# Performance work log

Hardware: AMD Instinct MI355X
Metric: run time of the kernel (lower is better)

The kernel has to match this reference:

```python
import jax, jax.numpy as jnp
import numpy as np

NUM_PAIRS, PAIR_DIM, MACRO_DIM, NUM_SLOTS, BATCH = 28, 128, 256, 64, 4096
D_ALL = NUM_PAIRS * PAIR_DIM  # 3584
EPS = 1e-5


def _layernorm(x, g, b):
    mu = jnp.mean(x, axis=-1, keepdims=True)
    var = jnp.mean(jnp.square(x - mu), axis=-1, keepdims=True)
    return (x - mu) * jax.lax.rsqrt(var + EPS) * g + b


def _memory_read(q, keys, values):
    # attention-style associative read: softmax(q K^T / sqrt(dk)) V
    dk = keys.shape[-1]
    scores = jnp.einsum('bd,sd->bs', q, keys) / jnp.sqrt(jnp.asarray(dk, q.dtype))
    attn = jax.nn.softmax(scores, axis=-1)
    return jnp.einsum('bs,sv->bv', attn, values)


def setup_inputs() -> dict:
    key = jax.random.key(0)
    ks = jax.random.split(key, 12)
    s = lambda k, shape, scale=0.02: jax.random.normal(k, shape, dtype=jnp.float32) * scale
    return {
        'pair_states': jax.random.normal(ks[0], (BATCH, NUM_PAIRS, PAIR_DIM), dtype=jnp.float32),
        'macro_state': jax.random.normal(ks[1], (BATCH, MACRO_DIM), dtype=jnp.float32),
        'mem_pair_keys': s(ks[2], (NUM_SLOTS, PAIR_DIM)),
        'mem_pair_vals': s(ks[3], (NUM_SLOTS, D_ALL)),
        'mem_macro_keys': s(ks[4], (NUM_SLOTS, MACRO_DIM)),
        'mem_macro_vals': s(ks[5], (NUM_SLOTS, D_ALL)),
        'fusion_w1': s(ks[6], (2 * D_ALL, D_ALL)),
        'fusion_b1': jnp.zeros((D_ALL,), jnp.float32),
        'fusion_ln_g': jnp.ones((D_ALL,), jnp.float32),
        'fusion_ln_b': jnp.zeros((D_ALL,), jnp.float32),
        'fusion_w2': s(ks[7], (D_ALL, D_ALL)),
        'fusion_b2': jnp.zeros((D_ALL,), jnp.float32),
        'pair_w': s(ks[8], (NUM_PAIRS, 2 * PAIR_DIM, PAIR_DIM)),
        'pair_b': jnp.zeros((NUM_PAIRS, PAIR_DIM), jnp.float32),
        'pair_ln_g': jnp.ones((NUM_PAIRS, PAIR_DIM), jnp.float32),
        'pair_ln_b': jnp.zeros((NUM_PAIRS, PAIR_DIM), jnp.float32),
    }


def reference(pair_states, macro_state, mem_pair_keys, mem_pair_vals,
              mem_macro_keys, mem_macro_vals, fusion_w1, fusion_b1,
              fusion_ln_g, fusion_ln_b, fusion_w2, fusion_b2,
              pair_w, pair_b, pair_ln_g, pair_ln_b):
    B = pair_states.shape[0]
    # associative memory reads
    pair_query = jnp.mean(pair_states, axis=1)                       # (B, pair_dim)
    pair_corr = _memory_read(pair_query, mem_pair_keys, mem_pair_vals)   # (B, D_ALL)
    macro_corr = _memory_read(macro_state, mem_macro_keys, mem_macro_vals)  # (B, D_ALL)
    # fusion MLP: Linear -> LayerNorm -> GELU -> Linear
    h = jnp.concatenate([pair_corr, macro_corr], axis=-1) @ fusion_w1 + fusion_b1
    h = jax.nn.gelu(_layernorm(h, fusion_ln_g, fusion_ln_b), approximate=False)
    fused = (h @ fusion_w2 + fusion_b2).reshape(B, NUM_PAIRS, PAIR_DIM)
    # per-pair Linear + LayerNorm, batched over the pair axis
    x = jnp.concatenate([pair_states, fused], axis=-1)               # (B, P, 2*pair_dim)
    out = jnp.einsum('bpd,pde->bpe', x, pair_w) + pair_b
    return _layernorm(out, pair_ln_g, pair_ln_b)
```

## Files before the change

### kernel.cpp

```cpp
#include <hip/hip_runtime.h>
#include <hip/hip_bf16.h>
#include <math.h>


#define B_SZ  4096
#define NPAIR 28
#define PDIM  128
#define MDIM  256
#define NSLOT 64
#define DALL  3584
#define DCAT  7168
#define KS2   16
#define KCH2  448

typedef __hip_bfloat16 bf16;
typedef __attribute__((ext_vector_type(8))) short bf16x8;
typedef __attribute__((ext_vector_type(4))) short short4v;
typedef __attribute__((ext_vector_type(4))) float f32x4;

#define BARRIER() asm volatile("s_barrier" ::: "memory")
#define LGKM0()   asm volatile("s_waitcnt lgkmcnt(0)" ::: "memory")
#define VMCNT4()  asm volatile("s_waitcnt vmcnt(4)" ::: "memory")
#define VMCNT0()  asm volatile("s_waitcnt vmcnt(0)" ::: "memory")

__device__ __forceinline__ void async_copy16(void* lds, const void* g) {
  __builtin_amdgcn_global_load_lds((__attribute__((address_space(1))) void*)g,
                                   (__attribute__((address_space(3))) void*)lds,
                                   16, 0, 0);
}

__global__ __launch_bounds__(512, 2)
void gemm224(const bf16* __restrict__ A, const bf16* __restrict__ Bt,
             bf16* __restrict__ Cout, const float* __restrict__ bias) {
  __shared__ __align__(16) char smem[131072];
  const int tid = threadIdx.x;
  const int wid = tid >> 6, lane = tid & 63;
  const int lr = lane & 15, lk = lane >> 4;
  const int wm = wid >> 1, wn = wid & 1;
  const int swz = ((int)blockIdx.x & 7) * 32 + ((int)blockIdx.x >> 3);
  const int bx = swz & 15, by = swz >> 4;
  const int col0 = bx * 224, row0 = by * 256;

  char* sA = smem;
  char* sB = smem + 65536;

  const int srow = tid >> 3;
  const int sg = (tid & 7) ^ (srow & 7);
  const bf16* aStage = A + (long)(row0 + srow) * DALL + sg * 8;
  const bf16* bStage = Bt + (long)(col0 + srow) * DALL + sg * 8;
  const int wOff = wid << 10;

  const int NT = DALL >> 6;

  const int sx = lr & 7;
  const int arowb = wm * 64 + lr;
  const int browb = wn * 112 + lr;

  f32x4 acc[4][7];
  const f32x4 zero = {0.f, 0.f, 0.f, 0.f};
#pragma unroll
  for (int m = 0; m < 4; ++m)
#pragma unroll
    for (int n = 0; n < 7; ++n) acc[m][n] = zero;

#pragma unroll
  for (int i = 0; i < 4; ++i)
    async_copy16(sB + i * 8192 + wOff, bStage + (long)i * 64 * DALL);
#pragma unroll
  for (int i = 0; i < 4; ++i)
    async_copy16(sA + i * 8192 + wOff, aStage + (long)i * 64 * DALL);
#pragma unroll
  for (int i = 0; i < 4; ++i)
    async_copy16(sB + 32768 + i * 8192 + wOff, bStage + (long)i * 64 * DALL + 64);
  VMCNT4();
  BARRIER();

  bf16x8 af[4][2], bf[7][2];

  for (int t = 0; t < NT; ++t) {
    const int cur = t & 1;
    char* cA = sA + cur * 32768;
    char* cB = sB + cur * 32768;
    char* nA = sA + (cur ^ 1) * 32768;

    if (t + 1 < NT) {
      const bf16* g = aStage + (long)(t + 1) * 64;
#pragma unroll
      for (int i = 0; i < 4; ++i)
        async_copy16(nA + i * 8192 + wOff, g + (long)i * 64 * DALL);
    }
#pragma unroll
    for (int m = 0; m < 4; ++m)
#pragma unroll
      for (int kk = 0; kk < 2; ++kk)
        af[m][kk] = *(const bf16x8*)(cA + (arowb + m * 16) * 128 +
                                     ((((kk << 2) | lk) ^ sx) << 4));
#pragma unroll
    for (int n = 0; n < 7; ++n)
#pragma unroll
      for (int kk = 0; kk < 2; ++kk)
        bf[n][kk] = *(const bf16x8*)(cB + (browb + n * 16) * 128 +
                                     ((((kk << 2) | lk) ^ sx) << 4));
    __builtin_amdgcn_s_setprio(1);
#pragma unroll
    for (int m = 0; m < 4; ++m)
#pragma unroll
      for (int n = 0; n < 4; ++n)
#pragma unroll
        for (int kk = 0; kk < 2; ++kk)
          acc[m][n] = __builtin_amdgcn_mfma_f32_16x16x32_bf16(
              af[m][kk], bf[n][kk], acc[m][n], 0, 0, 0);
    __builtin_amdgcn_s_setprio(0);
    LGKM0();
    BARRIER();

    const int more = (t + 2 < NT);
    if (more) {
      const bf16* g = bStage + (long)(t + 2) * 64;
#pragma unroll
      for (int i = 0; i < 4; ++i)
        async_copy16(cB + i * 8192 + wOff, g + (long)i * 64 * DALL);
    }
    __builtin_amdgcn_s_setprio(1);
#pragma unroll
    for (int m = 0; m < 4; ++m)
#pragma unroll
      for (int n = 4; n < 7; ++n)
#pragma unroll
        for (int kk = 0; kk < 2; ++kk)
          acc[m][n] = __builtin_amdgcn_mfma_f32_16x16x32_bf16(
              af[m][kk], bf[n][kk], acc[m][n], 0, 0, 0);
    __builtin_amdgcn_s_setprio(0);
    if (more) { VMCNT4(); } else { VMCNT0(); }
    BARRIER();
  }

#pragma unroll
  for (int m = 0; m < 4; ++m) {
#pragma unroll
    for (int n = 0; n < 7; ++n) {
      const int gc = col0 + wn * 112 + n * 16 + lr;
      const float bia = bias[gc];
#pragma unroll
      for (int j = 0; j < 4; ++j) {
        const int gr = row0 + wm * 64 + m * 16 + lk * 4 + j;
        Cout[(long)gr * DALL + gc] = __float2bfloat16(acc[m][n][j] + bia);
      }
    }
  }
}

__global__ __launch_bounds__(256)
void tconv_kernel(const float* __restrict__ in, bf16* __restrict__ out,
                  int R, int C, int inBatch, int outBatch) {
  __shared__ float tile[32][33];
  const int tid = threadIdx.x;
  const int tx = tid & 31, ty = tid >> 5;
  const long ib = (long)blockIdx.z * inBatch;
  const long ob = (long)blockIdx.z * outBatch;
  const int c0 = blockIdx.x * 32, r0 = blockIdx.y * 32;
#pragma unroll
  for (int i = 0; i < 4; ++i)
    tile[ty + i * 8][tx] = in[ib + (long)(r0 + ty + i * 8) * C + c0 + tx];
  __syncthreads();
  const int cl = tid >> 3, rq = (tid & 7) * 4;
  union { bf16 h[4]; short4v v; } u;
#pragma unroll
  for (int j = 0; j < 4; ++j) u.h[j] = __float2bfloat16(tile[rq + j][cl]);
  *(short4v*)(out + ob + (long)(c0 + cl) * R + r0 + rq) = u.v;
}

__global__ __launch_bounds__(256)
void conv2_kernel(const float* __restrict__ pv, const float* __restrict__ mv,
                  bf16* __restrict__ pvb, bf16* __restrict__ mvb) {
  const float* in = blockIdx.y ? mv : pv;
  bf16* out = blockIdx.y ? mvb : pvb;
  const int i = (blockIdx.x * 256 + threadIdx.x) * 8;
  float4 a = *(const float4*)(in + i);
  float4 b = *(const float4*)(in + i + 4);
  union { bf16 h[8]; bf16x8 v; } u;
  u.h[0] = __float2bfloat16(a.x); u.h[1] = __float2bfloat16(a.y);
  u.h[2] = __float2bfloat16(a.z); u.h[3] = __float2bfloat16(a.w);
  u.h[4] = __float2bfloat16(b.x); u.h[5] = __float2bfloat16(b.y);
  u.h[6] = __float2bfloat16(b.z); u.h[7] = __float2bfloat16(b.w);
  *(bf16x8*)(out + i) = u.v;
}

__global__ __launch_bounds__(256)
void prep_kernel(const float* __restrict__ ps, const float* __restrict__ mac,
                 const float* __restrict__ pkeys, const float* __restrict__ mkeys,
                 bf16* __restrict__ psb, bf16* __restrict__ att) {
  const int b = blockIdx.x, tid = threadIdx.x;
  __shared__ float q[PDIM];
  __shared__ float mrow[MDIM];
  __shared__ float red[16][PDIM];
  const float* prow = ps + (long)b * DALL;
  if (tid < MDIM) mrow[tid] = mac[(long)b * MDIM + tid];
  float a8[8];
#pragma unroll
  for (int j = 0; j < 8; ++j) a8[j] = 0.f;
  for (int i = tid * 8; i < DALL; i += 2048) {
    float4 a = *(const float4*)(prow + i);
    float4 c = *(const float4*)(prow + i + 4);
    union { bf16 h[8]; bf16x8 v; } u;
    u.h[0] = __float2bfloat16(a.x); u.h[1] = __float2bfloat16(a.y);
    u.h[2] = __float2bfloat16(a.z); u.h[3] = __float2bfloat16(a.w);
    u.h[4] = __float2bfloat16(c.x); u.h[5] = __float2bfloat16(c.y);
    u.h[6] = __float2bfloat16(c.z); u.h[7] = __float2bfloat16(c.w);
    *(bf16x8*)(psb + (long)b * DALL + i) = u.v;
    a8[0] += a.x; a8[1] += a.y; a8[2] += a.z; a8[3] += a.w;
    a8[4] += c.x; a8[5] += c.y; a8[6] += c.z; a8[7] += c.w;
  }
  {
    float* rp = &red[tid >> 4][(tid & 15) * 8];
    *(f32x4*)rp = *(f32x4*)&a8[0];
    *(f32x4*)(rp + 4) = *(f32x4*)&a8[4];
  }
  __syncthreads();
  if (tid < PDIM) {
    float s = 0.f;
#pragma unroll
    for (int k = 0; k < 16; ++k) s += red[k][tid];
    q[tid] = s * (1.f / NPAIR);
  }
  __syncthreads();
  const int wid = tid >> 6, lane = tid & 63;
  if (wid == 0) {
    float sc = 0.f;
    const float* kr = pkeys + lane * PDIM;
    for (int d = 0; d < PDIM; ++d) sc += q[d] * kr[d];
    sc *= 0.08838834764831845f;
    float mx = sc;
#pragma unroll
    for (int m = 32; m; m >>= 1) mx = fmaxf(mx, __shfl_xor(mx, m));
    float e = expf(sc - mx);
    float ssum = e;
#pragma unroll
    for (int m = 32; m; m >>= 1) ssum += __shfl_xor(ssum, m);
    att[(long)b * 128 + lane] = __float2bfloat16(e / ssum);
  } else if (wid == 1) {
    float sc = 0.f;
    const float* kr = mkeys + lane * MDIM;
    for (int d = 0; d < MDIM; ++d) sc += mrow[d] * kr[d];
    sc *= 0.0625f;
    float mx = sc;
#pragma unroll
    for (int m = 32; m; m >>= 1) mx = fmaxf(mx, __shfl_xor(mx, m));
    float e = expf(sc - mx);
    float ssum = e;
#pragma unroll
    for (int m = 32; m; m >>= 1) ssum += __shfl_xor(ssum, m);
    att[(long)b * 128 + 64 + lane] = __float2bfloat16(e / ssum);
  }
}

__global__ __launch_bounds__(256)
void precompute_direct(const float* __restrict__ w1, const bf16* __restrict__ pvb,
                       const bf16* __restrict__ mvb, float* __restrict__ part) {
  __shared__ __align__(16) bf16 sAt[256 * 40];
  __shared__ __align__(16) bf16 sBt[64 * 32];
  const int tid = threadIdx.x, wid = tid >> 6, lane = tid & 63;
  const int lr = lane & 15, lk = lane >> 4;
  const int n0 = blockIdx.x * 256;
  const int ksb = blockIdx.y;
  const int kbase = ksb * KCH2;
  const bf16* vb = (ksb < 8) ? pvb : mvb;
  const int kcol0 = (ksb < 8) ? kbase : kbase - DALL;

  const int bs = tid >> 2;
  const int bgs = (tid & 3) ^ (bs & 3);

  f32x4 acc[4][4];
  const f32x4 zero = {0.f, 0.f, 0.f, 0.f};
#pragma unroll
  for (int m = 0; m < 4; ++m)
#pragma unroll
    for (int n = 0; n < 4; ++n) acc[m][n] = zero;

  for (int kt = 0; kt < KCH2; kt += 32) {
    __syncthreads();
    {
      const float* src = w1 + (long)(kbase + kt) * DALL + n0 + tid;
      bf16* dst = sAt + tid * 40;
#pragma unroll
      for (int r8 = 0; r8 < 32; r8 += 4) {
        union { bf16 h[4]; short4v v; } u;
#pragma unroll
        for (int j = 0; j < 4; ++j)
          u.h[j] = __float2bfloat16(src[(long)(r8 + j) * DALL]);
        *(short4v*)(dst + r8) = u.v;
      }
    }
    async_copy16((char*)sBt + tid * 16,
                 vb + (long)bs * DALL + kcol0 + kt + bgs * 8);
    __syncthreads();
    bf16x8 af[4], bfr[4];
#pragma unroll
    for (int m = 0; m < 4; ++m)
      af[m] = *(const bf16x8*)((const char*)sAt +
                               ((wid * 64 + m * 16 + lr) * 40 + lk * 8) * 2);
#pragma unroll
    for (int n = 0; n < 4; ++n) {
      const int s = n * 16 + lr;
      bfr[n] = *(const bf16x8*)((const char*)sBt + s * 64 + ((lk ^ (s & 3)) << 4));
    }
#pragma unroll
    for (int m = 0; m < 4; ++m)
#pragma unroll
      for (int n = 0; n < 4; ++n)
        acc[m][n] =
            __builtin_amdgcn_mfma_f32_16x16x32_bf16(af[m], bfr[n], acc[m][n], 0, 0, 0);
  }
#pragma unroll
  for (int m = 0; m < 4; ++m)
#pragma unroll
    for (int n = 0; n < 4; ++n)
#pragma unroll
      for (int j = 0; j < 4; ++j) {
        const int gn = n0 + wid * 64 + m * 16 + lk * 4 + j;
        const int s = n * 16 + lr;
        part[((long)ksb * DALL + gn) * 64 + s] = acc[m][n][j];
      }
}

__global__ __launch_bounds__(256)
void reduce_cvt(const float* __restrict__ part, bf16* __restrict__ cvt) {
  const long i4 = ((long)blockIdx.x * 256 + threadIdx.x) * 4;
  const int n = (int)(i4 >> 7), sc = (int)(i4 & 127);
  const int half = sc >> 6, s0 = sc & 63;
  f32x4 s = {0.f, 0.f, 0.f, 0.f};
#pragma unroll
  for (int j = 0; j < 8; ++j)
    s += *(const f32x4*)(part + ((long)(half * 8 + j) * DALL + n) * 64 + s0);
#pragma unroll
  for (int k = 0; k < 4; ++k) cvt[i4 + k] = __float2bfloat16(s[k]);
}

__global__ __launch_bounds__(256)
void gemm_thin(const bf16* __restrict__ att, const bf16* __restrict__ cvt,
               bf16* __restrict__ hpre, const float* __restrict__ bias) {
  __shared__ __align__(16) bf16 sA[128 * 64];
  __shared__ __align__(16) bf16 sB[128 * 64];
  const int tid = threadIdx.x, wid = tid >> 6, lane = tid & 63;
  const int lr = lane & 15, lk = lane >> 4;
  const int col0 = blockIdx.x * 128, row0 = blockIdx.y * 128;
  const int srl = lane >> 3;
  const int sgl = (lane & 7) ^ srl;
  const int sx = lr & 7;

  f32x4 acc[2][8];
  const f32x4 zero = {0.f, 0.f, 0.f, 0.f};
#pragma unroll
  for (int m = 0; m < 2; ++m)
#pragma unroll
    for (int n = 0; n < 8; ++n) acc[m][n] = zero;

  for (int kt = 0; kt < 2; ++kt) {
    __syncthreads();
#pragma unroll
    for (int i = 0; i < 4; ++i) {
      const int r = i * 32 + wid * 8 + srl;
      async_copy16((char*)sA + i * 4096 + wid * 1024,
                   att + (long)(row0 + r) * 128 + kt * 64 + sgl * 8);
      async_copy16((char*)sB + i * 4096 + wid * 1024,
                   cvt + (long)(col0 + r) * 128 + kt * 64 + sgl * 8);
    }
    __syncthreads();
#pragma unroll
    for (int kk = 0; kk < 2; ++kk) {
      bf16x8 a0[2], b0[8];
      const int gb = (((kk << 2) | lk) ^ sx) << 4;
#pragma unroll
      for (int m = 0; m < 2; ++m)
        a0[m] = *(const bf16x8*)((const char*)sA + (wid * 32 + m * 16 + lr) * 128 + gb);
#pragma unroll
      for (int n = 0; n < 8; ++n)
        b0[n] = *(const bf16x8*)((const char*)sB + (n * 16 + lr) * 128 + gb);
#pragma unroll
      for (int m = 0; m < 2; ++m)
#pragma unroll
        for (int n = 0; n < 8; ++n)
          acc[m][n] = __builtin_amdgcn_mfma_f32_16x16x32_bf16(
              a0[m], b0[n], acc[m][n], 0, 0, 0);
    }
  }
#pragma unroll
  for (int m = 0; m < 2; ++m) {
#pragma unroll
    for (int n = 0; n < 8; ++n) {
      const int gc = col0 + n * 16 + lr;
      const float bia = bias[gc];
#pragma unroll
      for (int j = 0; j < 4; ++j) {
        const int gr = row0 + wid * 32 + m * 16 + lk * 4 + j;
        hpre[(long)gr * DALL + gc] = __float2bfloat16(acc[m][n][j] + bia);
      }
    }
  }
}

__global__ __launch_bounds__(256)
void ln_gelu_kernel(const bf16* __restrict__ h, const float* __restrict__ g,
                    const float* __restrict__ bb, bf16* __restrict__ h2) {
  const int row = blockIdx.x, tid = threadIdx.x;
  const bf16* x = h + (long)row * DALL;
  float v[14];
  float s1 = 0.f, s2 = 0.f;
#pragma unroll
  for (int i = 0; i < 14; ++i) {
    v[i] = __bfloat162float(x[i * 256 + tid]);
    s1 += v[i];
    s2 += v[i] * v[i];
  }
#pragma unroll
  for (int m = 32; m; m >>= 1) {
    s1 += __shfl_xor(s1, m);
    s2 += __shfl_xor(s2, m);
  }
  __shared__ float r1[4], r2[4];
  const int wid = tid >> 6, lane = tid & 63;
  if (lane == 0) {
    r1[wid] = s1;
    r2[wid] = s2;
  }
  __syncthreads();
  s1 = r1[0] + r1[1] + r1[2] + r1[3];
  s2 = r2[0] + r2[1] + r2[2] + r2[3];
  const float mean = s1 * (1.f / DALL);
  const float var = s2 * (1.f / DALL) - mean * mean;
  const float rstd = rsqrtf(var + 1e-5f);
#pragma unroll
  for (int i = 0; i < 14; ++i) {
    const int c = i * 256 + tid;
    const float y = (v[i] - mean) * rstd * g[c] + bb[c];
    const float ge = 0.5f * y * (1.f + erff(y * 0.7071067811865475f));
    h2[(long)row * DALL + c] = __float2bfloat16(ge);
  }
}

__global__ __launch_bounds__(256)
void pair_final(const bf16* __restrict__ psb, const bf16* __restrict__ fusedb,
                const bf16* __restrict__ pwT, const float* __restrict__ pb,
                const float* __restrict__ lng, const float* __restrict__ lnb,
                float* __restrict__ out) {
  __shared__ __align__(16) bf16 sA[128 * 64];
  __shared__ __align__(16) bf16 sB[128 * 64];
  const int tid = threadIdx.x, wid = tid >> 6, lane = tid & 63;
  const int lr = lane & 15, lk = lane >> 4;
  const int p = blockIdx.y, row0 = blockIdx.x * 128;
  const int srl = lane >> 3;
  const int sgl = (lane & 7) ^ srl;
  const int sx = lr & 7;
  const bf16* pwp = pwT + (long)p * (PDIM * MDIM);

  f32x4 acc[2][8];
  const f32x4 zero = {0.f, 0.f, 0.f, 0.f};
#pragma unroll
  for (int m = 0; m < 2; ++m)
#pragma unroll
    for (int n = 0; n < 8; ++n) acc[m][n] = zero;

  for (int kt = 0; kt < 4; ++kt) {
    __syncthreads();
    const bf16* Asrc = (kt < 2) ? psb : fusedb;
    const int acol = p * PDIM + (kt & 1) * 64;
#pragma unroll
    for (int i = 0; i < 4; ++i) {
      const int r = i * 32 + wid * 8 + srl;
      async_copy16((char*)sA + i * 4096 + wid * 1024,
                   Asrc + (long)(row0 + r) * DALL + acol + sgl * 8);
      async_copy16((char*)sB + i * 4096 + wid * 1024,
                   pwp + (long)r * MDIM + kt * 64 + sgl * 8);
    }
    __syncthreads();
#pragma unroll
    for (int kk = 0; kk < 2; ++kk) {
      bf16x8 a0[2], b0[8];
      const int gb = (((kk << 2) | lk) ^ sx) << 4;
#pragma unroll
      for (int m = 0; m < 2; ++m)
        a0[m] = *(const bf16x8*)((const char*)sA + (wid * 32 + m * 16 + lr) * 128 + gb);
#pragma unroll
      for (int n = 0; n < 8; ++n)
        b0[n] = *(const bf16x8*)((const char*)sB + (n * 16 + lr) * 128 + gb);
#pragma unroll
      for (int m = 0; m < 2; ++m)
#pragma unroll
        for (int n = 0; n < 8; ++n)
          acc[m][n] = __builtin_amdgcn_mfma_f32_16x16x32_bf16(
              a0[m], b0[n], acc[m][n], 0, 0, 0);
    }
  }
  float g_[8], b_[8], pb_[8];
#pragma unroll
  for (int n = 0; n < 8; ++n) {
    const int c = n * 16 + lr;
    g_[n] = lng[p * PDIM + c];
    b_[n] = lnb[p * PDIM + c];
    pb_[n] = pb[p * PDIM + c];
  }
#pragma unroll
  for (int m = 0; m < 2; ++m) {
#pragma unroll
    for (int j = 0; j < 4; ++j) {
      float vv[8];
      float s1 = 0.f, s2 = 0.f;
#pragma unroll
      for (int n = 0; n < 8; ++n) {
        vv[n] = acc[m][n][j] + pb_[n];
        s1 += vv[n];
        s2 += vv[n] * vv[n];
      }
#pragma unroll
      for (int msk = 1; msk <= 8; msk <<= 1) {
        s1 += __shfl_xor(s1, msk);
        s2 += __shfl_xor(s2, msk);
      }
      const float mean = s1 * (1.f / 128.f);
      const float var = s2 * (1.f / 128.f) - mean * mean;
      const float rstd = rsqrtf(var + 1e-5f);
      const int gr = row0 + wid * 32 + m * 16 + lk * 4 + j;
      float* orow = out + ((long)gr * NPAIR + p) * PDIM;
#pragma unroll
      for (int n = 0; n < 8; ++n)
        orow[n * 16 + lr] = (vv[n] - mean) * rstd * g_[n] + b_[n];
    }
  }
}

extern "C" void kernel_launch(void* const* d_in, const int* in_sizes, int n_in,
                              void* d_out, int out_size, void* d_ws, size_t ws_size,
                              hipStream_t stream) {
  (void)in_sizes; (void)n_in; (void)out_size; (void)ws_size;
  const float* ps   = (const float*)d_in[0];
  const float* mac  = (const float*)d_in[1];
  const float* pkey = (const float*)d_in[2];
  const float* pval = (const float*)d_in[3];
  const float* mkey = (const float*)d_in[4];
  const float* mval = (const float*)d_in[5];
  const float* w1   = (const float*)d_in[6];
  const float* b1   = (const float*)d_in[7];
  const float* lng1 = (const float*)d_in[8];
  const float* lnb1 = (const float*)d_in[9];
  const float* w2   = (const float*)d_in[10];
  const float* b2   = (const float*)d_in[11];
  const float* pw   = (const float*)d_in[12];
  const float* pb   = (const float*)d_in[13];
  const float* plng = (const float*)d_in[14];
  const float* plnb = (const float*)d_in[15];
  float* out = (float*)d_out;

  char* w = (char*)d_ws;
  size_t off = 0;
  auto carve = [&](size_t bytes) {
    char* pp = w + off;
    off += (bytes + 255) & ~(size_t)255;
    return pp;
  };
  bf16* psb   = (bf16*)carve((size_t)B_SZ * DALL * 2);
  bf16* w2t   = (bf16*)carve((size_t)(DALL + 32) * DALL * 2);
  bf16* pvb   = (bf16*)carve((size_t)NSLOT * DALL * 2);
  bf16* mvb   = (bf16*)carve((size_t)NSLOT * DALL * 2);
  bf16* pwTb  = (bf16*)carve((size_t)NPAIR * PDIM * MDIM * 2);
  bf16* att   = (bf16*)carve((size_t)B_SZ * 128 * 2);
  bf16* cvt   = (bf16*)carve((size_t)DALL * 128 * 2);
  float* part = (float*)carve((size_t)KS2 * DALL * 64 * 4);
  bf16* hpreb = (bf16*)carve((size_t)B_SZ * DALL * 2);
  bf16* h2    = (bf16*)carve((size_t)B_SZ * DALL * 2);
  bf16* fusedb = hpreb;

  conv2_kernel<<<dim3(NSLOT * DALL / 2048, 2), 256, 0, stream>>>(pval, mval, pvb, mvb);
  tconv_kernel<<<dim3(DALL / 32, DALL / 32, 1), 256, 0, stream>>>(w2, w2t, DALL, DALL, 0, 0);
  tconv_kernel<<<dim3(PDIM / 32, MDIM / 32, NPAIR), 256, 0, stream>>>(
      pw, pwTb, MDIM, PDIM, MDIM * PDIM, MDIM * PDIM);
  prep_kernel<<<dim3(B_SZ), 256, 0, stream>>>(ps, mac, pkey, mkey, psb, att);
  precompute_direct<<<dim3(DALL / 256, KS2), 256, 0, stream>>>(w1, pvb, mvb, part);
  reduce_cvt<<<dim3(DALL * 128 / 1024), 256, 0, stream>>>(part, cvt);
  gemm_thin<<<dim3(DALL / 128, B_SZ / 128), 256, 0, stream>>>(att, cvt, hpreb, b1);
  ln_gelu_kernel<<<dim3(B_SZ), 256, 0, stream>>>(hpreb, lng1, lnb1, h2);
  gemm224<<<dim3(256), 512, 0, stream>>>(h2, w2t, fusedb, b2);
  pair_final<<<dim3(B_SZ / 128, NPAIR), 256, 0, stream>>>(
      psb, fusedb, pwTb, pb, plng, plnb, out);
}
```

Before: 280.3 us.

## Fuse thin GEMM with LayerNorm and GELU in one row-block kernel

Merges the K=128 thin GEMM and the LayerNorm+GELU pass into one kernel. Each block owns 16 rows, computes all 3584 columns with MFMA straight from global-memory fragments, stages the pre-activation in about 115 KB of LDS, then normalizes and writes h2. This removes the write and re-read of the 4096x3584 bf16 pre-activation and one kernel launch. In exchange it uses large LDS per block (low occupancy), only 256 blocks, and reloads the cvt matrix from global for every block without LDS staging.

```diff
diff --git a/kernel.cpp b/kernel.cpp
--- a/kernel.cpp
+++ b/kernel.cpp
@@ -12,6 +12,7 @@
 #define DCAT  7168
 #define KS2   16
 #define KCH2  448
+#define HCOLS 3600
 
 typedef __hip_bfloat16 bf16;
 typedef __attribute__((ext_vector_type(8))) short bf16x8;
@@ -337,104 +338,94 @@
 }
 
 __global__ __launch_bounds__(256)
-void gemm_thin(const bf16* __restrict__ att, const bf16* __restrict__ cvt,
-               bf16* __restrict__ hpre, const float* __restrict__ bias) {
-  __shared__ __align__(16) bf16 sA[128 * 64];
-  __shared__ __align__(16) bf16 sB[128 * 64];
+void fused_mlp1(const bf16* __restrict__ att, const bf16* __restrict__ cvt,
+                const float* __restrict__ b1, const float* __restrict__ g,
+                const float* __restrict__ bb, bf16* __restrict__ h2) {
+  __shared__ __align__(16) bf16 sH[16 * HCOLS];
+  __shared__ float sred[4][16][2];
   const int tid = threadIdx.x, wid = tid >> 6, lane = tid & 63;
   const int lr = lane & 15, lk = lane >> 4;
-  const int col0 = blockIdx.x * 128, row0 = blockIdx.y * 128;
-  const int srl = lane >> 3;
-  const int sgl = (lane & 7) ^ srl;
-  const int sx = lr & 7;
-
-  f32x4 acc[2][8];
+  const int r0 = blockIdx.x * 16;
+  const int c0 = wid * 896;
+
+  bf16x8 af[4];
+#pragma unroll
+  for (int ks = 0; ks < 4; ++ks)
+    af[ks] = *(const bf16x8*)(att + (long)(r0 + lr) * 128 + ks * 32 + lk * 8);
+
+  float s1[4], s2[4];
+#pragma unroll
+  for (int j = 0; j < 4; ++j) { s1[j] = 0.f; s2[j] = 0.f; }
+
   const f32x4 zero = {0.f, 0.f, 0.f, 0.f};
 #pragma unroll
-  for (int m = 0; m < 2; ++m)
-#pragma unroll
-    for (int n = 0; n < 8; ++n) acc[m][n] = zero;
-
-  for (int kt = 0; kt < 2; ++kt) {
-    __syncthreads();
-#pragma unroll
-    for (int i = 0; i < 4; ++i) {
-      const int r = i * 32 + wid * 8 + srl;
-      async_copy16((char*)sA + i * 4096 + wid * 1024,
-                   att + (long)(row0 + r) * 128 + kt * 64 + sgl * 8);
-      async_copy16((char*)sB + i * 4096 + wid * 1024,
-                   cvt + (long)(col0 + r) * 128 + kt * 64 + sgl * 8);
-    }
-    __syncthreads();
-#pragma unroll
-    for (int kk = 0; kk < 2; ++kk) {
-      bf16x8 a0[2], b0[8];
-      const int gb = (((kk << 2) | lk) ^ sx) << 4;
-#pragma unroll
-      for (int m = 0; m < 2; ++m)
-        a0[m] = *(const bf16x8*)((const char*)sA + (wid * 32 + m * 16 + lr) * 128 + gb);
-#pragma unroll
-      for (int n = 0; n < 8; ++n)
-        b0[n] = *(const bf16x8*)((const char*)sB + (n * 16 + lr) * 128 + gb);
-#pragma unroll
-      for (int m = 0; m < 2; ++m)
-#pragma unroll
-        for (int n = 0; n < 8; ++n)
-          acc[m][n] = __builtin_amdgcn_mfma_f32_16x16x32_bf16(
-              a0[m], b0[n], acc[m][n], 0, 0, 0);
-    }
-  }
-#pragma unroll
-  for (int m = 0; m < 2; ++m) {
-#pragma unroll
-    for (int n = 0; n < 8; ++n) {
-      const int gc = col0 + n * 16 + lr;
-      const float bia = bias[gc];
+  for (int half = 0; half < 2; ++half) {
+    const int hc0 = c0 + half * 448;
+    f32x4 acc[28];
+#pragma unroll
+    for (int n = 0; n < 28; ++n) acc[n] = zero;
+#pragma unroll
+    for (int ks = 0; ks < 4; ++ks)
+#pragma unroll
+      for (int n = 0; n < 28; ++n) {
+        bf16x8 bfr = *(const bf16x8*)(cvt + (long)(hc0 + n * 16 + lr) * 128 +
+                                      ks * 32 + lk * 8);
+        acc[n] = __builtin_amdgcn_mfma_f32_16x16x32_bf16(af[ks], bfr, acc[n], 0, 0, 0);
+      }
+#pragma unroll
+    for (int n = 0; n < 28; ++n) {
+      const int col = hc0 + n * 16 + lr;
+      const float bia = b1[col];
 #pragma unroll
       for (int j = 0; j < 4; ++j) {
-        const int gr = row0 + wid * 32 + m * 16 + lk * 4 + j;
-        hpre[(long)gr * DALL + gc] = __float2bfloat16(acc[m][n][j] + bia);
-      }
-    }
-  }
-}
-
-__global__ __launch_bounds__(256)
-void ln_gelu_kernel(const bf16* __restrict__ h, const float* __restrict__ g,
-                    const float* __restrict__ bb, bf16* __restrict__ h2) {
-  const int row = blockIdx.x, tid = threadIdx.x;
-  const bf16* x = h + (long)row * DALL;
-  float v[14];
-  float s1 = 0.f, s2 = 0.f;
-#pragma unroll
-  for (int i = 0; i < 14; ++i) {
-    v[i] = __bfloat162float(x[i * 256 + tid]);
-    s1 += v[i];
-    s2 += v[i] * v[i];
-  }
-#pragma unroll
-  for (int m = 32; m; m >>= 1) {
-    s1 += __shfl_xor(s1, m);
-    s2 += __shfl_xor(s2, m);
-  }
-  __shared__ float r1[4], r2[4];
-  const int wid = tid >> 6, lane = tid & 63;
-  if (lane == 0) {
-    r1[wid] = s1;
-    r2[wid] = s2;
+        const float v = acc[n][j] + bia;
+        s1[j] += v;
+        s2[j] += v * v;
+        sH[(lk * 4 + j) * HCOLS + col] = __float2bfloat16(v);
+      }
+    }
+  }
+#pragma unroll
+  for (int j = 0; j < 4; ++j) {
+#pragma unroll
+    for (int msk = 1; msk <= 8; msk <<= 1) {
+      s1[j] += __shfl_xor(s1[j], msk);
+      s2[j] += __shfl_xor(s2[j], msk);
+    }
+  }
+  if (lr == 0) {
+#pragma unroll
+    for (int j = 0; j < 4; ++j) {
+      sred[wid][lk * 4 + j][0] = s1[j];
+      sred[wid][lk * 4 + j][1] = s2[j];
+    }
   }
   __syncthreads();
-  s1 = r1[0] + r1[1] + r1[2] + r1[3];
-  s2 = r2[0] + r2[1] + r2[2] + r2[3];
-  const float mean = s1 * (1.f / DALL);
-  const float var = s2 * (1.f / DALL) - mean * mean;
+  const int row = tid >> 4, cb = (tid & 15) * 8;
+  float t1 = 0.f, t2 = 0.f;
+#pragma unroll
+  for (int w = 0; w < 4; ++w) { t1 += sred[w][row][0]; t2 += sred[w][row][1]; }
+  const float mean = t1 * (1.f / DALL);
+  const float var = t2 * (1.f / DALL) - mean * mean;
   const float rstd = rsqrtf(var + 1e-5f);
-#pragma unroll
-  for (int i = 0; i < 14; ++i) {
-    const int c = i * 256 + tid;
-    const float y = (v[i] - mean) * rstd * g[c] + bb[c];
-    const float ge = 0.5f * y * (1.f + erff(y * 0.7071067811865475f));
-    h2[(long)row * DALL + c] = __float2bfloat16(ge);
+  bf16* orow = h2 + (long)(r0 + row) * DALL;
+#pragma unroll
+  for (int c = cb; c < DALL; c += 128) {
+    bf16x8 hv = *(const bf16x8*)(sH + row * HCOLS + c);
+    float4 g0 = *(const float4*)(g + c);
+    float4 g1 = *(const float4*)(g + c + 4);
+    float4 b0 = *(const float4*)(bb + c);
+    float4 b1v = *(const float4*)(bb + c + 4);
+    const float gg[8] = {g0.x, g0.y, g0.z, g0.w, g1.x, g1.y, g1.z, g1.w};
+    const float bbv[8] = {b0.x, b0.y, b0.z, b0.w, b1v.x, b1v.y, b1v.z, b1v.w};
+    union { bf16 hh[8]; bf16x8 vv; } u;
+#pragma unroll
+    for (int j = 0; j < 8; ++j) {
+      const float x = __bfloat162float(((const bf16*)&hv)[j]);
+      const float y = (x - mean) * rstd * gg[j] + bbv[j];
+      u.hh[j] = __float2bfloat16(0.5f * y * (1.f + erff(y * 0.7071067811865475f)));
+    }
+    *(bf16x8*)(orow + c) = u.vv;
   }
 }
 
@@ -565,9 +556,8 @@
   bf16* att   = (bf16*)carve((size_t)B_SZ * 128 * 2);
   bf16* cvt   = (bf16*)carve((size_t)DALL * 128 * 2);
   float* part = (float*)carve((size_t)KS2 * DALL * 64 * 4);
-  bf16* hpreb = (bf16*)carve((size_t)B_SZ * DALL * 2);
   bf16* h2    = (bf16*)carve((size_t)B_SZ * DALL * 2);
-  bf16* fusedb = hpreb;
+  bf16* fusedb = (bf16*)carve((size_t)B_SZ * DALL * 2);
 
   conv2_kernel<<<dim3(NSLOT * DALL / 2048, 2), 256, 0, stream>>>(pval, mval, pvb, mvb);
   tconv_kernel<<<dim3(DALL / 32, DALL / 32, 1), 256, 0, stream>>>(w2, w2t, DALL, DALL, 0, 0);
@@ -576,8 +566,7 @@
   prep_kernel<<<dim3(B_SZ), 256, 0, stream>>>(ps, mac, pkey, mkey, psb, att);
   precompute_direct<<<dim3(DALL / 256, KS2), 256, 0, stream>>>(w1, pvb, mvb, part);
   reduce_cvt<<<dim3(DALL * 128 / 1024), 256, 0, stream>>>(part, cvt);
-  gemm_thin<<<dim3(DALL / 128, B_SZ / 128), 256, 0, stream>>>(att, cvt, hpreb, b1);
-  ln_gelu_kernel<<<dim3(B_SZ), 256, 0, stream>>>(hpreb, lng1, lnb1, h2);
+  fused_mlp1<<<dim3(B_SZ / 16), 256, 0, stream>>>(att, cvt, b1, lng1, lnb1, h2);
   gemm224<<<dim3(256), 512, 0, stream>>>(h2, w2t, fusedb, b2);
   pair_final<<<dim3(B_SZ / 128, NPAIR), 256, 0, stream>>>(
       psb, fusedb, pwTb, pb, plng, plnb, out);
```

After: 302.9 us. 8.1% more time.
